# Kernel optimization log

Hardware: AMD Instinct MI355X
Metric: run time of the kernel (lower is better)

The kernel has to match this reference:

```python
import jax, jax.numpy as jnp
import numpy as np

NUM_FEATURES = 512
NUM_HID = 16
NUM_CLASSES = 40


def _glorot(key, shape):
    lim = float(np.sqrt(6.0 / (shape[0] + shape[1])))
    return jax.random.uniform(key, shape, jnp.float32, -lim, lim)


def setup_inputs() -> dict:
    key = jax.random.key(0)
    k1, k2, k3, k4 = jax.random.split(key, 4)
    N, E = 100000, 3200000
    x = jax.random.normal(k1, (N, NUM_FEATURES), jnp.float32)
    edge_index = jax.random.randint(k2, (2, E), 0, N, jnp.int64)
    W1 = _glorot(k3, (NUM_FEATURES, NUM_HID))
    b1 = jnp.zeros((NUM_HID,), jnp.float32)
    W2 = _glorot(k4, (NUM_HID, NUM_CLASSES))
    b2 = jnp.zeros((NUM_CLASSES,), jnp.float32)
    return {"x": x, "edge_index": edge_index, "num_nodes": N,
            "W1": W1, "b1": b1, "W2": W2, "b2": b2}


def gcn_conv(x, src, dst, norm, W, b, num_nodes):
    # linear transform first (PyG GCNConv), then normalized scatter-add
    h = x @ W                                    # [N, out]
    msg = h[src] * norm[:, None]                 # [E+N, out]
    agg = jax.ops.segment_sum(msg, dst, num_segments=num_nodes)
    return agg + b


def reference(x, edge_index, num_nodes, W1, b1, W2, b2):
    # add self-loops and compute symmetric normalization deg^-1/2 A_hat deg^-1/2
    loops = jnp.arange(num_nodes, dtype=edge_index.dtype)
    src = jnp.concatenate([edge_index[0], loops])
    dst = jnp.concatenate([edge_index[1], loops])
    ones = jnp.ones(src.shape, x.dtype)
    deg = jax.ops.segment_sum(ones, dst, num_segments=num_nodes)
    dinv = jnp.where(deg > 0, deg ** -0.5, 0.0)
    norm = dinv[src] * dinv[dst]

    h = jax.nn.relu(gcn_conv(x, src, dst, norm, W1, b1, num_nodes))
    # dropout omitted: inference mode (training=False)
    h = gcn_conv(h, src, dst, norm, W2, b2, num_nodes)
    out = jax.nn.softmax(h, axis=1)
    return (out, h)
```

## Files before the change

### kernel.cpp

```cpp
#include <hip/hip_runtime.h>
#include <math.h>

#define F 512
#define H 16
#define C 40
#define BW 128
#define BSH 7
#define NB_MAX 1024
#define CHUNK 4096
#define EPT 16
#define SRC_BITS 17
#define SRC_MASK 0x1FFFF
#define SORT_CAP 8192

__global__ __launch_bounds__(256) void k_scatfuse(const int* __restrict__ src,
                                                  const int* __restrict__ dst,
                                                  int* __restrict__ gcnt,
                                                  int* __restrict__ ebuf, int E, int NB) {
    __shared__ int hist[NB_MAX];
    __shared__ int base2[NB_MAX];
    __shared__ int cur[NB_MAX];
    __shared__ int tsum[256];
    __shared__ int paddr[CHUNK];
    __shared__ int pdata[CHUNK];
    int c = blockIdx.x, t = threadIdx.x;
    int i0 = c * CHUNK;
    int nval = min(CHUNK, E - i0);
    for (int b = t; b < NB; b += 256) hist[b] = 0;
    const int4* s4 = (const int4*)(src + i0);
    const int4* d4 = (const int4*)(dst + i0);
    int dreg[EPT], sreg[EPT];
    #pragma unroll
    for (int j = 0; j < EPT / 4; j++) {
        int i4 = t + j * 256;
        int base = i4 * 4;
        if (base + 3 < nval) {
            int4 dv = d4[i4], sv = s4[i4];
            dreg[j*4+0] = dv.x; dreg[j*4+1] = dv.y; dreg[j*4+2] = dv.z; dreg[j*4+3] = dv.w;
            sreg[j*4+0] = sv.x; sreg[j*4+1] = sv.y; sreg[j*4+2] = sv.z; sreg[j*4+3] = sv.w;
        } else {
            #pragma unroll
            for (int k = 0; k < 4; k++) {
                int idx = base + k;
                if (idx < nval) { dreg[j*4+k] = dst[i0 + idx]; sreg[j*4+k] = src[i0 + idx]; }
                else dreg[j*4+k] = -1;
            }
        }
    }
    __syncthreads();
    #pragma unroll
    for (int j = 0; j < EPT; j++)
        if (dreg[j] >= 0) atomicAdd(&hist[dreg[j] >> BSH], 1);
    __syncthreads();
    int b0 = t * 4;
    int v0 = (b0 + 0 < NB) ? hist[b0 + 0] : 0;
    int v1 = (b0 + 1 < NB) ? hist[b0 + 1] : 0;
    int v2 = (b0 + 2 < NB) ? hist[b0 + 2] : 0;
    int v3 = (b0 + 3 < NB) ? hist[b0 + 3] : 0;
    int loc1 = v0, loc2 = v0 + v1, loc3 = v0 + v1 + v2;
    int s = loc3 + v3;
    tsum[t] = s;
    __syncthreads();
    for (int off = 1; off < 256; off <<= 1) {
        int v = (t >= off) ? tsum[t - off] : 0;
        __syncthreads();
        tsum[t] += v;
        __syncthreads();
    }
    int excl = tsum[t] - s;
    if (b0 + 0 < NB) { int p = excl;        cur[b0+0] = p; int g = v0 ? atomicAdd(&gcnt[b0+0], v0) : 0; base2[b0+0] = (b0+0)*SORT_CAP + g - p; }
    if (b0 + 1 < NB) { int p = excl + loc1; cur[b0+1] = p; int g = v1 ? atomicAdd(&gcnt[b0+1], v1) : 0; base2[b0+1] = (b0+1)*SORT_CAP + g - p; }
    if (b0 + 2 < NB) { int p = excl + loc2; cur[b0+2] = p; int g = v2 ? atomicAdd(&gcnt[b0+2], v2) : 0; base2[b0+2] = (b0+2)*SORT_CAP + g - p; }
    if (b0 + 3 < NB) { int p = excl + loc3; cur[b0+3] = p; int g = v3 ? atomicAdd(&gcnt[b0+3], v3) : 0; base2[b0+3] = (b0+3)*SORT_CAP + g - p; }
    __syncthreads();
    #pragma unroll
    for (int j = 0; j < EPT; j++) {
        int d = dreg[j];
        if (d < 0) continue;
        int b = d >> BSH;
        int r = atomicAdd(&cur[b], 1);
        paddr[r] = base2[b] + r;
        pdata[r] = ((d & (BW - 1)) << SRC_BITS) | sreg[j];
    }
    __syncthreads();
    for (int i = t; i < nval; i += 256)
        ebuf[paddr[i]] = pdata[i];
}

__global__ __launch_bounds__(256) void k_sortb(int* __restrict__ ebuf,
                                               const int* __restrict__ gcnt,
                                               int2* __restrict__ rowbe,
                                               float* __restrict__ dinv, int N) {
    __shared__ int out[SORT_CAP];
    __shared__ int hist[BW];
    __shared__ int off[BW];
    __shared__ int cur[BW];
    int b = blockIdx.x;
    int beg = b * SORT_CAP;
    int len = gcnt[b];
    if (len > SORT_CAP) len = SORT_CAP;
    int tid = threadIdx.x;
    if (tid < BW) hist[tid] = 0;
    __syncthreads();
    int len4 = len >> 2;
    const int4* e4 = (const int4*)(ebuf + beg);
    for (int i = tid; i < len4; i += 256) {
        int4 w = e4[i];
        atomicAdd(&hist[w.x >> SRC_BITS], 1);
        atomicAdd(&hist[w.y >> SRC_BITS], 1);
        atomicAdd(&hist[w.z >> SRC_BITS], 1);
        atomicAdd(&hist[w.w >> SRC_BITS], 1);
    }
    for (int i = (len4 << 2) + tid; i < len; i += 256)
        atomicAdd(&hist[ebuf[beg + i] >> SRC_BITS], 1);
    __syncthreads();
    if (tid < BW) off[tid] = hist[tid];
    __syncthreads();
    for (int d = 1; d < BW; d <<= 1) {
        int v = (tid < BW && tid >= d) ? off[tid - d] : 0;
        __syncthreads();
        if (tid < BW) off[tid] += v;
        __syncthreads();
    }
    if (tid < BW) {
        int excl = off[tid] - hist[tid];
        int n = b * BW + tid;
        if (n < N) {
            rowbe[n] = make_int2(beg + excl, beg + off[tid]);
            dinv[n] = rsqrtf((float)(hist[tid] + 1));
        }
        cur[tid] = excl;
    }
    __syncthreads();
    for (int i = tid; i < len4; i += 256) {
        int4 w = e4[i];
        int r0 = atomicAdd(&cur[w.x >> SRC_BITS], 1);
        int r1 = atomicAdd(&cur[w.y >> SRC_BITS], 1);
        int r2 = atomicAdd(&cur[w.z >> SRC_BITS], 1);
        int r3 = atomicAdd(&cur[w.w >> SRC_BITS], 1);
        out[r0] = w.x & SRC_MASK;
        out[r1] = w.y & SRC_MASK;
        out[r2] = w.z & SRC_MASK;
        out[r3] = w.w & SRC_MASK;
    }
    for (int i = (len4 << 2) + tid; i < len; i += 256) {
        int w = ebuf[beg + i];
        int r = atomicAdd(&cur[w >> SRC_BITS], 1);
        out[r] = w & SRC_MASK;
    }
    __syncthreads();
    int n4 = (len + 3) >> 2;
    int4* o4 = (int4*)(ebuf + beg);
    const int4* p4 = (const int4*)out;
    for (int i = tid; i < n4; i += 256) o4[i] = p4[i];
}

#define KT 64
#define GST 68
__global__ __launch_bounds__(64) void k_gemm1(const float* __restrict__ x,
                                              const float* __restrict__ W1,
                                              const float* __restrict__ dinv,
                                              float* __restrict__ h0s, int N) {
    __shared__ float xs[64 * GST];
    int t = threadIdx.x;
    int n0 = blockIdx.x * 64;
    float acc[H];
    #pragma unroll
    for (int j = 0; j < H; j++) acc[j] = 0.f;
    for (int kt = 0; kt < F; kt += KT) {
        __syncthreads();
        #pragma unroll
        for (int p = 0; p < 16; p++) {
            int idx = t + (p << 6);
            int r = idx >> 4, c4 = idx & 15;
            int v = n0 + r; if (v >= N) v = N - 1;
            float4 val = *(const float4*)(x + (size_t)v * F + kt + (c4 << 2));
            *(float4*)&xs[r * GST + (c4 << 2)] = val;
        }
        __syncthreads();
        #pragma unroll
        for (int k4 = 0; k4 < 16; k4++) {
            float4 xv = *(const float4*)&xs[t * GST + (k4 << 2)];
            const float* w = W1 + (size_t)(kt + (k4 << 2)) * H;
            #pragma unroll
            for (int j = 0; j < H; j++) acc[j] = fmaf(xv.x, w[j], acc[j]);
            #pragma unroll
            for (int j = 0; j < H; j++) acc[j] = fmaf(xv.y, w[H + j], acc[j]);
            #pragma unroll
            for (int j = 0; j < H; j++) acc[j] = fmaf(xv.z, w[2 * H + j], acc[j]);
            #pragma unroll
            for (int j = 0; j < H; j++) acc[j] = fmaf(xv.w, w[3 * H + j], acc[j]);
        }
    }
    int v = n0 + t;
    if (v >= N) return;
    float dv = dinv[v];
    float4* o4 = (float4*)(h0s + (size_t)v * H);
    o4[0] = make_float4(acc[0] * dv, acc[1] * dv, acc[2] * dv, acc[3] * dv);
    o4[1] = make_float4(acc[4] * dv, acc[5] * dv, acc[6] * dv, acc[7] * dv);
    o4[2] = make_float4(acc[8] * dv, acc[9] * dv, acc[10] * dv, acc[11] * dv);
    o4[3] = make_float4(acc[12] * dv, acc[13] * dv, acc[14] * dv, acc[15] * dv);
}

__global__ __launch_bounds__(256) void k_agg1(const float* __restrict__ hs,
                                              const int* __restrict__ adj,
                                              const int2* __restrict__ rowbe,
                                              const float* __restrict__ dinv,
                                              const float* __restrict__ b1,
                                              float* __restrict__ out, int N) {
    int t = blockIdx.x * 256 + threadIdx.x;
    int n = t >> 2, q = t & 3;
    if (n >= N) return;
    const float4* hs4 = (const float4*)hs;
    int2 be = rowbe[n];
    int beg = be.x, end = be.y;
    float4 a = hs4[(size_t)n * 4 + q];
    float ax = a.x, ay = a.y, az = a.z, aw = a.w;
    int e = beg;
    for (; e + 7 < end; e += 8) {
        int s0 = adj[e], s1 = adj[e + 1], s2 = adj[e + 2], s3 = adj[e + 3];
        int s4 = adj[e + 4], s5 = adj[e + 5], s6 = adj[e + 6], s7 = adj[e + 7];
        float4 v0 = hs4[(size_t)s0 * 4 + q];
        float4 v1 = hs4[(size_t)s1 * 4 + q];
        float4 v2 = hs4[(size_t)s2 * 4 + q];
        float4 v3 = hs4[(size_t)s3 * 4 + q];
        float4 v4 = hs4[(size_t)s4 * 4 + q];
        float4 v5 = hs4[(size_t)s5 * 4 + q];
        float4 v6 = hs4[(size_t)s6 * 4 + q];
        float4 v7 = hs4[(size_t)s7 * 4 + q];
        ax += ((v0.x + v1.x) + (v2.x + v3.x)) + ((v4.x + v5.x) + (v6.x + v7.x));
        ay += ((v0.y + v1.y) + (v2.y + v3.y)) + ((v4.y + v5.y) + (v6.y + v7.y));
        az += ((v0.z + v1.z) + (v2.z + v3.z)) + ((v4.z + v5.z) + (v6.z + v7.z));
        aw += ((v0.w + v1.w) + (v2.w + v3.w)) + ((v4.w + v5.w) + (v6.w + v7.w));
    }
    for (; e + 3 < end; e += 4) {
        int s0 = adj[e], s1 = adj[e + 1], s2 = adj[e + 2], s3 = adj[e + 3];
        float4 v0 = hs4[(size_t)s0 * 4 + q];
        float4 v1 = hs4[(size_t)s1 * 4 + q];
        float4 v2 = hs4[(size_t)s2 * 4 + q];
        float4 v3 = hs4[(size_t)s3 * 4 + q];
        ax += (v0.x + v1.x) + (v2.x + v3.x);
        ay += (v0.y + v1.y) + (v2.y + v3.y);
        az += (v0.z + v1.z) + (v2.z + v3.z);
        aw += (v0.w + v1.w) + (v2.w + v3.w);
    }
    for (; e < end; e++) {
        int s = adj[e];
        float4 v = hs4[(size_t)s * 4 + q];
        ax += v.x; ay += v.y; az += v.z; aw += v.w;
    }
    float dv = dinv[n];
    float4 r;
    r.x = fmaxf(fmaf(dv, ax, b1[q * 4 + 0]), 0.f) * dv;
    r.y = fmaxf(fmaf(dv, ay, b1[q * 4 + 1]), 0.f) * dv;
    r.z = fmaxf(fmaf(dv, az, b1[q * 4 + 2]), 0.f) * dv;
    r.w = fmaxf(fmaf(dv, aw, b1[q * 4 + 3]), 0.f) * dv;
    ((float4*)out)[(size_t)n * 4 + q] = r;
}

__global__ __launch_bounds__(256) void k_agg2out(const float* __restrict__ hs,
                                                 const int* __restrict__ adj,
                                                 const int2* __restrict__ rowbe,
                                                 const float* __restrict__ dinv,
                                                 const float* __restrict__ W2,
                                                 const float* __restrict__ b2,
                                                 float* __restrict__ dout, int N) {
    __shared__ float sg[64 * 16];
    __shared__ float w2s[H * C];
    __shared__ float b2s[C];
    __shared__ float so[64 * 40];
    int t = threadIdx.x;
    for (int i = t; i < H * C; i += 256) w2s[i] = W2[i];
    if (t < C) b2s[t] = b2[t];
    int nl = t >> 2, q = t & 3;
    int n0 = blockIdx.x * 64;
    int n = n0 + nl;
    bool valid = (n < N);
    int nn = valid ? n : N - 1;
    const float4* hs4 = (const float4*)hs;
    int2 be = rowbe[nn];
    int beg = be.x, end = be.y;
    float4 a = hs4[(size_t)nn * 4 + q];
    float ax = a.x, ay = a.y, az = a.z, aw = a.w;
    int e = beg;
    for (; e + 7 < end; e += 8) {
        int s0 = adj[e], s1 = adj[e + 1], s2 = adj[e + 2], s3 = adj[e + 3];
        int s4 = adj[e + 4], s5 = adj[e + 5], s6 = adj[e + 6], s7 = adj[e + 7];
        float4 v0 = hs4[(size_t)s0 * 4 + q];
        float4 v1 = hs4[(size_t)s1 * 4 + q];
        float4 v2 = hs4[(size_t)s2 * 4 + q];
        float4 v3 = hs4[(size_t)s3 * 4 + q];
        float4 v4 = hs4[(size_t)s4 * 4 + q];
        float4 v5 = hs4[(size_t)s5 * 4 + q];
        float4 v6 = hs4[(size_t)s6 * 4 + q];
        float4 v7 = hs4[(size_t)s7 * 4 + q];
        ax += ((v0.x + v1.x) + (v2.x + v3.x)) + ((v4.x + v5.x) + (v6.x + v7.x));
        ay += ((v0.y + v1.y) + (v2.y + v3.y)) + ((v4.y + v5.y) + (v6.y + v7.y));
        az += ((v0.z + v1.z) + (v2.z + v3.z)) + ((v4.z + v5.z) + (v6.z + v7.z));
        aw += ((v0.w + v1.w) + (v2.w + v3.w)) + ((v4.w + v5.w) + (v6.w + v7.w));
    }
    for (; e + 3 < end; e += 4) {
        int s0 = adj[e], s1 = adj[e + 1], s2 = adj[e + 2], s3 = adj[e + 3];
        float4 v0 = hs4[(size_t)s0 * 4 + q];
        float4 v1 = hs4[(size_t)s1 * 4 + q];
        float4 v2 = hs4[(size_t)s2 * 4 + q];
        float4 v3 = hs4[(size_t)s3 * 4 + q];
        ax += (v0.x + v1.x) + (v2.x + v3.x);
        ay += (v0.y + v1.y) + (v2.y + v3.y);
        az += (v0.z + v1.z) + (v2.z + v3.z);
        aw += (v0.w + v1.w) + (v2.w + v3.w);
    }
    for (; e < end; e++) {
        int s = adj[e];
        float4 v = hs4[(size_t)s * 4 + q];
        ax += v.x; ay += v.y; az += v.z; aw += v.w;
    }
    float dv = dinv[nn];
    *(float4*)&sg[nl * 16 + q * 4] = make_float4(dv * ax, dv * ay, dv * az, dv * aw);
    __syncthreads();
    float g16[16];
    #pragma unroll
    for (int k4 = 0; k4 < 4; k4++) {
        float4 gv = *(const float4*)&sg[nl * 16 + k4 * 4];
        g16[k4 * 4] = gv.x; g16[k4 * 4 + 1] = gv.y;
        g16[k4 * 4 + 2] = gv.z; g16[k4 * 4 + 3] = gv.w;
    }
    int j0 = q * 10;
    float h2[10];
    #pragma unroll
    for (int jj = 0; jj < 10; jj++) {
        float acc = b2s[j0 + jj];
        #pragma unroll
        for (int k = 0; k < H; k++) acc = fmaf(g16[k], w2s[k * C + j0 + jj], acc);
        h2[jj] = acc;
    }
    float m = h2[0];
    #pragma unroll
    for (int jj = 1; jj < 10; jj++) m = fmaxf(m, h2[jj]);
    m = fmaxf(m, __shfl_xor(m, 1, 64));
    m = fmaxf(m, __shfl_xor(m, 2, 64));
    float ex[10], ssum = 0.f;
    #pragma unroll
    for (int jj = 0; jj < 10; jj++) { ex[jj] = __expf(h2[jj] - m); ssum += ex[jj]; }
    ssum += __shfl_xor(ssum, 1, 64);
    ssum += __shfl_xor(ssum, 2, 64);
    float inv = 1.f / ssum;
    int rows = min(64, N - n0);
    int tot = rows * 10;
    #pragma unroll
    for (int jj = 0; jj < 10; jj++) so[nl * 40 + j0 + jj] = ex[jj] * inv;
    __syncthreads();
    {
        const float4* sp4 = (const float4*)so;
        float4* o4 = (float4*)(dout + (size_t)n0 * C);
        for (int i = t; i < tot; i += 256) o4[i] = sp4[i];
    }
    __syncthreads();
    #pragma unroll
    for (int jj = 0; jj < 10; jj++) so[nl * 40 + j0 + jj] = h2[jj];
    __syncthreads();
    {
        const float4* sp4 = (const float4*)so;
        float4* o4 = (float4*)(dout + (size_t)N * C + (size_t)n0 * C);
        for (int i = t; i < tot; i += 256) o4[i] = sp4[i];
    }
}

extern "C" void kernel_launch(void* const* d_in, const int* in_sizes, int n_in,
                              void* d_out, int out_size, void* d_ws, size_t ws_size,
                              hipStream_t stream) {
    const float* x  = (const float*)d_in[0];
    const int*   ei = (const int*)d_in[1];
    const float* W1 = (const float*)d_in[3];
    const float* b1 = (const float*)d_in[4];
    const float* W2 = (const float*)d_in[5];
    const float* b2 = (const float*)d_in[6];
    float* out = (float*)d_out;

    int N = in_sizes[0] / F;
    int E = in_sizes[1] / 2;
    const int* src = ei;
    const int* dst = ei + E;
    int NB  = (N + BW - 1) / BW;
    int NCH = (E + CHUNK - 1) / CHUNK;

    float* ws = (float*)d_ws;
    size_t o = 0;
    int* gcnt  = (int*)(ws + o); o += (size_t)NB_MAX;
    int2* rowbe = (int2*)(ws + o); o += 2 * ((size_t)N + 4);
    o = (o + 3) & ~(size_t)3;
    int* ebuf  = (int*)(ws + o); o += (size_t)NB * SORT_CAP + CHUNK;
    float* dinv = ws + o;        o += (size_t)N;
    float* h0s  = ws + o;        o += (size_t)N * H;
    float* h1s  = ws + o;        o += (size_t)N * H;

    int ng = (N + 63) / 64;

    hipMemsetAsync(gcnt, 0, (size_t)NB * sizeof(int), stream);
    k_scatfuse<<<NCH, 256, 0, stream>>>(src, dst, gcnt, ebuf, E, NB);
    k_sortb   <<<NB, 256, 0, stream>>>(ebuf, gcnt, rowbe, dinv, N);
    k_gemm1   <<<ng, 64, 0, stream>>>(x, W1, dinv, h0s, N);
    k_agg1    <<<(N * 4 + 255) / 256, 256, 0, stream>>>(h0s, ebuf, rowbe, dinv, b1, h1s, N);
    k_agg2out <<<ng, 256, 0, stream>>>(h1s, ebuf, rowbe, dinv, W2, b2, out, N);
}
```

Measured before the change: 530.3 us.

## Run edge scatter and first GEMM concurrently in one fused front kernel

Merges the edge-bucketing scatter and the x@W1 projection into one launch, where the block index chooses the role, so the bandwidth-heavy GEMM over x overlaps with the atomic-heavy scatter. Because dinv is not yet known when the GEMM runs, the deg^-1/2 scaling of h0s moves into the sort kernel, which rescales each node's row in place after computing its degree. The GEMM part now runs four 64-row wavefronts per block with a 32-wide K tile. The cost is an extra read-modify-write pass over h0s and shared-memory sizing set by the scatter role, which may limit occupancy of the GEMM blocks.

```diff
diff --git a/kernel.cpp b/kernel.cpp
--- a/kernel.cpp
+++ b/kernel.cpp
@@ -13,88 +13,140 @@
 #define SRC_MASK 0x1FFFF
 #define SORT_CAP 8192
 
-__global__ __launch_bounds__(256) void k_scatfuse(const int* __restrict__ src,
-                                                  const int* __restrict__ dst,
-                                                  int* __restrict__ gcnt,
-                                                  int* __restrict__ ebuf, int E, int NB) {
-    __shared__ int hist[NB_MAX];
-    __shared__ int base2[NB_MAX];
-    __shared__ int cur[NB_MAX];
-    __shared__ int tsum[256];
-    __shared__ int paddr[CHUNK];
-    __shared__ int pdata[CHUNK];
-    int c = blockIdx.x, t = threadIdx.x;
-    int i0 = c * CHUNK;
-    int nval = min(CHUNK, E - i0);
-    for (int b = t; b < NB; b += 256) hist[b] = 0;
-    const int4* s4 = (const int4*)(src + i0);
-    const int4* d4 = (const int4*)(dst + i0);
-    int dreg[EPT], sreg[EPT];
-    #pragma unroll
-    for (int j = 0; j < EPT / 4; j++) {
-        int i4 = t + j * 256;
-        int base = i4 * 4;
-        if (base + 3 < nval) {
-            int4 dv = d4[i4], sv = s4[i4];
-            dreg[j*4+0] = dv.x; dreg[j*4+1] = dv.y; dreg[j*4+2] = dv.z; dreg[j*4+3] = dv.w;
-            sreg[j*4+0] = sv.x; sreg[j*4+1] = sv.y; sreg[j*4+2] = sv.z; sreg[j*4+3] = sv.w;
-        } else {
+#define KT2 32
+#define GST2 36
+__global__ __launch_bounds__(256) void k_front(const int* __restrict__ src,
+                                               const int* __restrict__ dst,
+                                               int* __restrict__ gcnt,
+                                               int* __restrict__ ebuf,
+                                               const float* __restrict__ x,
+                                               const float* __restrict__ W1,
+                                               float* __restrict__ h0s,
+                                               int E, int NB, int N, int NCH) {
+    __shared__ int smem[11520];
+    int t = threadIdx.x;
+    if ((int)blockIdx.x < NCH) {
+        int* paddr = smem;
+        int* pdata = smem + 4096;
+        int* hist  = smem + 8192;
+        int* base2 = smem + 9216;
+        int* cur   = smem + 10240;
+        int* tsum  = smem + 11264;
+        int c = blockIdx.x;
+        int i0 = c * CHUNK;
+        int nval = min(CHUNK, E - i0);
+        for (int b = t; b < NB; b += 256) hist[b] = 0;
+        const int4* s4 = (const int4*)(src + i0);
+        const int4* d4 = (const int4*)(dst + i0);
+        int dreg[EPT], sreg[EPT];
+        #pragma unroll
+        for (int j = 0; j < EPT / 4; j++) {
+            int i4 = t + j * 256;
+            int base = i4 * 4;
+            if (base + 3 < nval) {
+                int4 dv = d4[i4], sv = s4[i4];
+                dreg[j*4+0] = dv.x; dreg[j*4+1] = dv.y; dreg[j*4+2] = dv.z; dreg[j*4+3] = dv.w;
+                sreg[j*4+0] = sv.x; sreg[j*4+1] = sv.y; sreg[j*4+2] = sv.z; sreg[j*4+3] = sv.w;
+            } else {
+                #pragma unroll
+                for (int k = 0; k < 4; k++) {
+                    int idx = base + k;
+                    if (idx < nval) { dreg[j*4+k] = dst[i0 + idx]; sreg[j*4+k] = src[i0 + idx]; }
+                    else dreg[j*4+k] = -1;
+                }
+            }
+        }
+        __syncthreads();
+        #pragma unroll
+        for (int j = 0; j < EPT; j++)
+            if (dreg[j] >= 0) atomicAdd(&hist[dreg[j] >> BSH], 1);
+        __syncthreads();
+        int b0 = t * 4;
+        int v0 = (b0 + 0 < NB) ? hist[b0 + 0] : 0;
+        int v1 = (b0 + 1 < NB) ? hist[b0 + 1] : 0;
+        int v2 = (b0 + 2 < NB) ? hist[b0 + 2] : 0;
+        int v3 = (b0 + 3 < NB) ? hist[b0 + 3] : 0;
+        int loc1 = v0, loc2 = v0 + v1, loc3 = v0 + v1 + v2;
+        int s = loc3 + v3;
+        tsum[t] = s;
+        __syncthreads();
+        for (int off = 1; off < 256; off <<= 1) {
+            int v = (t >= off) ? tsum[t - off] : 0;
+            __syncthreads();
+            tsum[t] += v;
+            __syncthreads();
+        }
+        int excl = tsum[t] - s;
+        if (b0 + 0 < NB) { int p = excl;        cur[b0+0] = p; int g = v0 ? atomicAdd(&gcnt[b0+0], v0) : 0; base2[b0+0] = (b0+0)*SORT_CAP + g - p; }
+        if (b0 + 1 < NB) { int p = excl + loc1; cur[b0+1] = p; int g = v1 ? atomicAdd(&gcnt[b0+1], v1) : 0; base2[b0+1] = (b0+1)*SORT_CAP + g - p; }
+        if (b0 + 2 < NB) { int p = excl + loc2; cur[b0+2] = p; int g = v2 ? atomicAdd(&gcnt[b0+2], v2) : 0; base2[b0+2] = (b0+2)*SORT_CAP + g - p; }
+        if (b0 + 3 < NB) { int p = excl + loc3; cur[b0+3] = p; int g = v3 ? atomicAdd(&gcnt[b0+3], v3) : 0; base2[b0+3] = (b0+3)*SORT_CAP + g - p; }
+        __syncthreads();
+        #pragma unroll
+        for (int j = 0; j < EPT; j++) {
+            int d = dreg[j];
+            if (d < 0) continue;
+            int b = d >> BSH;
+            int r = atomicAdd(&cur[b], 1);
+            paddr[r] = base2[b] + r;
+            pdata[r] = ((d & (BW - 1)) << SRC_BITS) | sreg[j];
+        }
+        __syncthreads();
+        for (int i = t; i < nval; i += 256)
+            ebuf[paddr[i]] = pdata[i];
+    } else {
+        int g = blockIdx.x - NCH;
+        int w = t >> 6, lane = t & 63;
+        float* xs = (float*)smem + w * (64 * GST2);
+        int n0 = g * 256 + w * 64;
+        float acc[H];
+        #pragma unroll
+        for (int j = 0; j < H; j++) acc[j] = 0.f;
+        for (int kt = 0; kt < F; kt += KT2) {
+            __syncthreads();
             #pragma unroll
-            for (int k = 0; k < 4; k++) {
-                int idx = base + k;
-                if (idx < nval) { dreg[j*4+k] = dst[i0 + idx]; sreg[j*4+k] = src[i0 + idx]; }
-                else dreg[j*4+k] = -1;
+            for (int p = 0; p < 8; p++) {
+                int idx = lane + (p << 6);
+                int r = idx >> 3, c4 = idx & 7;
+                int v = n0 + r; if (v >= N) v = N - 1;
+                float4 val = *(const float4*)(x + (size_t)v * F + kt + (c4 << 2));
+                *(float4*)&xs[r * GST2 + (c4 << 2)] = val;
             }
-        }
-    }
-    __syncthreads();
-    #pragma unroll
-    for (int j = 0; j < EPT; j++)
-        if (dreg[j] >= 0) atomicAdd(&hist[dreg[j] >> BSH], 1);
-    __syncthreads();
-    int b0 = t * 4;
-    int v0 = (b0 + 0 < NB) ? hist[b0 + 0] : 0;
-    int v1 = (b0 + 1 < NB) ? hist[b0 + 1] : 0;
-    int v2 = (b0 + 2 < NB) ? hist[b0 + 2] : 0;
-    int v3 = (b0 + 3 < NB) ? hist[b0 + 3] : 0;
-    int loc1 = v0, loc2 = v0 + v1, loc3 = v0 + v1 + v2;
-    int s = loc3 + v3;
-    tsum[t] = s;
-    __syncthreads();
-    for (int off = 1; off < 256; off <<= 1) {
-        int v = (t >= off) ? tsum[t - off] : 0;
-        __syncthreads();
-        tsum[t] += v;
-        __syncthreads();
-    }
-    int excl = tsum[t] - s;
-    if (b0 + 0 < NB) { int p = excl;        cur[b0+0] = p; int g = v0 ? atomicAdd(&gcnt[b0+0], v0) : 0; base2[b0+0] = (b0+0)*SORT_CAP + g - p; }
-    if (b0 + 1 < NB) { int p = excl + loc1; cur[b0+1] = p; int g = v1 ? atomicAdd(&gcnt[b0+1], v1) : 0; base2[b0+1] = (b0+1)*SORT_CAP + g - p; }
-    if (b0 + 2 < NB) { int p = excl + loc2; cur[b0+2] = p; int g = v2 ? atomicAdd(&gcnt[b0+2], v2) : 0; base2[b0+2] = (b0+2)*SORT_CAP + g - p; }
-    if (b0 + 3 < NB) { int p = excl + loc3; cur[b0+3] = p; int g = v3 ? atomicAdd(&gcnt[b0+3], v3) : 0; base2[b0+3] = (b0+3)*SORT_CAP + g - p; }
-    __syncthreads();
-    #pragma unroll
-    for (int j = 0; j < EPT; j++) {
-        int d = dreg[j];
-        if (d < 0) continue;
-        int b = d >> BSH;
-        int r = atomicAdd(&cur[b], 1);
-        paddr[r] = base2[b] + r;
-        pdata[r] = ((d & (BW - 1)) << SRC_BITS) | sreg[j];
-    }
-    __syncthreads();
-    for (int i = t; i < nval; i += 256)
-        ebuf[paddr[i]] = pdata[i];
+            __syncthreads();
+            #pragma unroll
+            for (int k4 = 0; k4 < 8; k4++) {
+                float4 xv = *(const float4*)&xs[lane * GST2 + (k4 << 2)];
+                const float* wp = W1 + (size_t)(kt + (k4 << 2)) * H;
+                #pragma unroll
+                for (int j = 0; j < H; j++) acc[j] = fmaf(xv.x, wp[j], acc[j]);
+                #pragma unroll
+                for (int j = 0; j < H; j++) acc[j] = fmaf(xv.y, wp[H + j], acc[j]);
+                #pragma unroll
+                for (int j = 0; j < H; j++) acc[j] = fmaf(xv.z, wp[2 * H + j], acc[j]);
+                #pragma unroll
+                for (int j = 0; j < H; j++) acc[j] = fmaf(xv.w, wp[3 * H + j], acc[j]);
+            }
+        }
+        int v = n0 + lane;
+        if (v >= N) return;
+        float4* o4 = (float4*)(h0s + (size_t)v * H);
+        o4[0] = make_float4(acc[0], acc[1], acc[2], acc[3]);
+        o4[1] = make_float4(acc[4], acc[5], acc[6], acc[7]);
+        o4[2] = make_float4(acc[8], acc[9], acc[10], acc[11]);
+        o4[3] = make_float4(acc[12], acc[13], acc[14], acc[15]);
+    }
 }
 
 __global__ __launch_bounds__(256) void k_sortb(int* __restrict__ ebuf,
                                                const int* __restrict__ gcnt,
                                                int2* __restrict__ rowbe,
-                                               float* __restrict__ dinv, int N) {
+                                               float* __restrict__ dinv,
+                                               float* __restrict__ h0s, int N) {
     __shared__ int out[SORT_CAP];
     __shared__ int hist[BW];
     __shared__ int off[BW];
     __shared__ int cur[BW];
+    __shared__ float dloc[BW];
     int b = blockIdx.x;
     int beg = b * SORT_CAP;
     int len = gcnt[b];
@@ -125,13 +177,26 @@
     if (tid < BW) {
         int excl = off[tid] - hist[tid];
         int n = b * BW + tid;
+        float dv = rsqrtf((float)(hist[tid] + 1));
+        dloc[tid] = dv;
         if (n < N) {
             rowbe[n] = make_int2(beg + excl, beg + off[tid]);
-            dinv[n] = rsqrtf((float)(hist[tid] + 1));
+            dinv[n] = dv;
         }
         cur[tid] = excl;
     }
     __syncthreads();
+    {
+        int nl = tid >> 1, hf = tid & 1;
+        int n = b * BW + nl;
+        if (n < N) {
+            float dv = dloc[nl];
+            float4* p = (float4*)(h0s + (size_t)n * H + hf * 8);
+            float4 a = p[0], c = p[1];
+            p[0] = make_float4(a.x * dv, a.y * dv, a.z * dv, a.w * dv);
+            p[1] = make_float4(c.x * dv, c.y * dv, c.z * dv, c.w * dv);
+        }
+    }
     for (int i = tid; i < len4; i += 256) {
         int4 w = e4[i];
         int r0 = atomicAdd(&cur[w.x >> SRC_BITS], 1);
@@ -153,53 +218,6 @@
     int4* o4 = (int4*)(ebuf + beg);
     const int4* p4 = (const int4*)out;
     for (int i = tid; i < n4; i += 256) o4[i] = p4[i];
-}
-
-#define KT 64
-#define GST 68
-__global__ __launch_bounds__(64) void k_gemm1(const float* __restrict__ x,
-                                              const float* __restrict__ W1,
-                                              const float* __restrict__ dinv,
-                                              float* __restrict__ h0s, int N) {
-    __shared__ float xs[64 * GST];
-    int t = threadIdx.x;
-    int n0 = blockIdx.x * 64;
-    float acc[H];
-    #pragma unroll
-    for (int j = 0; j < H; j++) acc[j] = 0.f;
-    for (int kt = 0; kt < F; kt += KT) {
-        __syncthreads();
-        #pragma unroll
-        for (int p = 0; p < 16; p++) {
-            int idx = t + (p << 6);
-            int r = idx >> 4, c4 = idx & 15;
-            int v = n0 + r; if (v >= N) v = N - 1;
-            float4 val = *(const float4*)(x + (size_t)v * F + kt + (c4 << 2));
-            *(float4*)&xs[r * GST + (c4 << 2)] = val;
-        }
-        __syncthreads();
-        #pragma unroll
-        for (int k4 = 0; k4 < 16; k4++) {
-            float4 xv = *(const float4*)&xs[t * GST + (k4 << 2)];
-            const float* w = W1 + (size_t)(kt + (k4 << 2)) * H;
-            #pragma unroll
-            for (int j = 0; j < H; j++) acc[j] = fmaf(xv.x, w[j], acc[j]);
-            #pragma unroll
-            for (int j = 0; j < H; j++) acc[j] = fmaf(xv.y, w[H + j], acc[j]);
-            #pragma unroll
-            for (int j = 0; j < H; j++) acc[j] = fmaf(xv.z, w[2 * H + j], acc[j]);
-            #pragma unroll
-            for (int j = 0; j < H; j++) acc[j] = fmaf(xv.w, w[3 * H + j], acc[j]);
-        }
-    }
-    int v = n0 + t;
-    if (v >= N) return;
-    float dv = dinv[v];
-    float4* o4 = (float4*)(h0s + (size_t)v * H);
-    o4[0] = make_float4(acc[0] * dv, acc[1] * dv, acc[2] * dv, acc[3] * dv);
-    o4[1] = make_float4(acc[4] * dv, acc[5] * dv, acc[6] * dv, acc[7] * dv);
-    o4[2] = make_float4(acc[8] * dv, acc[9] * dv, acc[10] * dv, acc[11] * dv);
-    o4[3] = make_float4(acc[12] * dv, acc[13] * dv, acc[14] * dv, acc[15] * dv);
 }
 
 __global__ __launch_bounds__(256) void k_agg1(const float* __restrict__ hs,
@@ -383,6 +401,7 @@
     const int* dst = ei + E;
     int NB  = (N + BW - 1) / BW;
     int NCH = (E + CHUNK - 1) / CHUNK;
+    int NG4 = (N + 255) / 256;
 
     float* ws = (float*)d_ws;
     size_t o = 0;
@@ -397,9 +416,8 @@
     int ng = (N + 63) / 64;
 
     hipMemsetAsync(gcnt, 0, (size_t)NB * sizeof(int), stream);
-    k_scatfuse<<<NCH, 256, 0, stream>>>(src, dst, gcnt, ebuf, E, NB);
-    k_sortb   <<<NB, 256, 0, stream>>>(ebuf, gcnt, rowbe, dinv, N);
-    k_gemm1   <<<ng, 64, 0, stream>>>(x, W1, dinv, h0s, N);
+    k_front   <<<NCH + NG4, 256, 0, stream>>>(src, dst, gcnt, ebuf, x, W1, h0s, E, NB, N, NCH);
+    k_sortb   <<<NB, 256, 0, stream>>>(ebuf, gcnt, rowbe, dinv, h0s, N);
     k_agg1    <<<(N * 4 + 255) / 256, 256, 0, stream>>>(h0s, ebuf, rowbe, dinv, b1, h1s, N);
     k_agg2out <<<ng, 256, 0, stream>>>(h1s, ebuf, rowbe, dinv, W2, b2, out, N);
 }
```

Measured after the change: 519.0 us. -2.1%, faster.
